# Kernel optimization log

Measured on AMD Instinct MI355X. Metric: run time of the kernel, lower is better.

Reference implementation:

```python
import jax, jax.numpy as jnp
import numpy as np

HS, FF, NH = 1024, 4096, 16
HD = HS // NH
EPS = 1e-5

def _ln(x, g, b):
    m = jnp.mean(x, axis=-1, keepdims=True)
    v = jnp.mean((x - m) ** 2, axis=-1, keepdims=True)
    return (x - m) * jax.lax.rsqrt(v + EPS) * g + b

def setup_inputs() -> dict:
    key = jax.random.key(0)
    ks = jax.random.split(key, 12)
    s = 1.0 / np.sqrt(HS)
    si = 1.0 / np.sqrt(FF)
    d = {
        "hidden_states": jax.random.normal(ks[0], (2, 2048, HS), dtype=jnp.float32),
        "attention_mask": jnp.zeros((2, 1, 1, 2048), dtype=jnp.float32),
        "Wq": jax.random.uniform(ks[1], (HS, HS), minval=-s, maxval=s),
        "bq": jnp.zeros((HS,), jnp.float32),
        "Wk": jax.random.uniform(ks[2], (HS, HS), minval=-s, maxval=s),
        "bk": jnp.zeros((HS,), jnp.float32),
        "Wv": jax.random.uniform(ks[3], (HS, HS), minval=-s, maxval=s),
        "bv": jnp.zeros((HS,), jnp.float32),
        "Wo": jax.random.uniform(ks[4], (HS, HS), minval=-s, maxval=s),
        "bo": jnp.zeros((HS,), jnp.float32),
        "W1": jax.random.uniform(ks[5], (HS, FF), minval=-s, maxval=s),
        "b1": jnp.zeros((FF,), jnp.float32),
        "W2": jax.random.uniform(ks[6], (FF, HS), minval=-si, maxval=si),
        "b2": jnp.zeros((HS,), jnp.float32),
        "ln1_g": jnp.ones((HS,), jnp.float32),
        "ln1_b": jnp.zeros((HS,), jnp.float32),
        "ln2_g": jnp.ones((HS,), jnp.float32),
        "ln2_b": jnp.zeros((HS,), jnp.float32),
    }
    return d

def reference(hidden_states, attention_mask, Wq, bq, Wk, bk, Wv, bv, Wo, bo,
              W1, b1, W2, b2, ln1_g, ln1_b, ln2_g, ln2_b):
    bs, S, _ = hidden_states.shape
    x = hidden_states
    # self-attention (dropout is identity in eval)
    q = (x @ Wq + bq).reshape(bs, S, NH, HD).transpose(0, 2, 1, 3)
    k = (x @ Wk + bk).reshape(bs, S, NH, HD).transpose(0, 2, 1, 3)
    v = (x @ Wv + bv).reshape(bs, S, NH, HD).transpose(0, 2, 1, 3)
    scores = jnp.einsum("bhqd,bhkd->bhqk", q, k) / np.sqrt(HD) + attention_mask
    probs = jax.nn.softmax(scores, axis=-1)
    attn = jnp.einsum("bhqk,bhkd->bhqd", probs, v)
    attn = attn.transpose(0, 2, 1, 3).reshape(bs, S, HS)
    mha = attn @ Wo + bo
    h = _ln(x + mha, ln1_g, ln1_b)
    # FFN
    ff = jax.nn.relu(h @ W1 + b1) @ W2 + b2
    return _ln(h + ff, ln2_g, ln2_b)
```

## Files before the change

kernel.cpp:

```cpp
#include <hip/hip_runtime.h>
#include <hip/hip_bf16.h>

#define HS   1024
#define FF   4096
#define NH   16
#define HD   64
#define SEQ  2048
#define BSZ  2
#define MROWS (BSZ * SEQ)
#define EPS  1e-5f
#define QKV_STRIDE (3 * HS)

typedef float f32x4  __attribute__((ext_vector_type(4)));
typedef short bf16x8 __attribute__((ext_vector_type(8)));

__device__ __forceinline__ unsigned short f2bf(float x) {
  unsigned int u = __float_as_uint(x);
  u += 0x7fffu + ((u >> 16) & 1u);
  return (unsigned short)(u >> 16);
}

__device__ __forceinline__ unsigned int pkbf(float a, float b) {
  union { __hip_bfloat162 h; unsigned int u; } x;
  x.h = __float22bfloat162_rn(float2{a, b});
  return x.u;
}

__device__ __forceinline__ void async16(const ushort* g, ushort* lds) {
  __builtin_amdgcn_global_load_lds(
      (const __attribute__((address_space(1))) unsigned int*)g,
      (__attribute__((address_space(3))) unsigned int*)lds, 16, 0, 0);
}

template <int TBM, int TBN, bool RELU, bool OUT_BF16, bool PARTIAL>
__global__ __launch_bounds__(256) void gemm_bf16_kernel(
    const ushort* __restrict__ A, const ushort* __restrict__ Bt,
    const float* __restrict__ bias, void* __restrict__ Cout,
    int M, int N, int K, int kLen, size_t zstride)
{
  constexpr int MI = TBM / 32;
  constexpr int NJ = TBN / 32;
  __shared__ ushort As[TBM * 64];
  __shared__ ushort Bs[TBN * 64];

  const int tid = threadIdx.x;
  const int wv = tid >> 6, ln = tid & 63;
  const int bn = blockIdx.x, bm = blockIdx.y;

  const int lr = ln & 15;
  const int lg = ln >> 4;
  const int mrow_base = (wv >> 1) * (TBM / 2);
  const int ncol_base = (wv & 1) * (TBN / 2);

  f32x4 acc[MI][NJ];
#pragma unroll
  for (int i = 0; i < MI; ++i)
#pragma unroll
    for (int j = 0; j < NJ; ++j) acc[i][j] = (f32x4){0.f, 0.f, 0.f, 0.f};

  const int rr = ln >> 3, cc = ln & 7;
  const int kBeg = blockIdx.z * kLen, kEnd = kBeg + kLen;

  for (int k0 = kBeg; k0 < kEnd; k0 += 64) {
    __syncthreads();
#pragma unroll
    for (int t = 0; t < TBM / 32; ++t) {
      const int R = wv * (TBM / 4) + t * 8 + rr;
      const int c = cc ^ (R & 7);
      async16(A + (size_t)(bm * TBM + R) * K + k0 + c * 8,
              &As[(size_t)(wv * (TBM / 4) + t * 8) * 64]);
    }
#pragma unroll
    for (int t = 0; t < TBN / 32; ++t) {
      const int R = wv * (TBN / 4) + t * 8 + rr;
      const int c = cc ^ (R & 7);
      async16(Bt + (size_t)(bn * TBN + R) * K + k0 + c * 8,
              &Bs[(size_t)(wv * (TBN / 4) + t * 8) * 64]);
    }
    __syncthreads();

#pragma unroll
    for (int s = 0; s < 2; ++s) {
      bf16x8 a[MI], b[NJ];
#pragma unroll
      for (int i = 0; i < MI; ++i) {
        const int m = mrow_base + i * 16 + lr;
        a[i] = *(const bf16x8*)&As[(size_t)m * 64 + (((s * 4 + lg) ^ (m & 7)) * 8)];
      }
#pragma unroll
      for (int j = 0; j < NJ; ++j) {
        const int n = ncol_base + j * 16 + lr;
        b[j] = *(const bf16x8*)&Bs[(size_t)n * 64 + (((s * 4 + lg) ^ (n & 7)) * 8)];
      }
#pragma unroll
      for (int i = 0; i < MI; ++i)
#pragma unroll
        for (int j = 0; j < NJ; ++j)
          acc[i][j] = __builtin_amdgcn_mfma_f32_16x16x32_bf16(a[i], b[j], acc[i][j], 0, 0, 0);
    }
  }

  const int gm0 = bm * TBM + mrow_base;
  const int gn0 = bn * TBN + ncol_base;

  if (PARTIAL) {
    float* Cp = (float*)Cout + (size_t)blockIdx.z * zstride;
#pragma unroll
    for (int i = 0; i < MI; ++i)
#pragma unroll
      for (int r = 0; r < 4; ++r) {
        const size_t row = (size_t)(gm0 + i * 16 + lg * 4 + r);
#pragma unroll
        for (int j = 0; j < NJ; ++j)
          Cp[row * N + gn0 + j * 16 + lr] = acc[i][j][r];
      }
  } else {
    float bs4[NJ];
#pragma unroll
    for (int j = 0; j < NJ; ++j) bs4[j] = bias[gn0 + j * 16 + lr];
    float* Cf = (float*)Cout;
    ushort* Cb = (ushort*)Cout;
#pragma unroll
    for (int i = 0; i < MI; ++i) {
#pragma unroll
      for (int r = 0; r < 4; ++r) {
        const size_t row = (size_t)(gm0 + i * 16 + lg * 4 + r);
#pragma unroll
        for (int j = 0; j < NJ; ++j) {
          float val = acc[i][j][r] + bs4[j];
          if (RELU) val = fmaxf(val, 0.f);
          const size_t idx = row * N + gn0 + j * 16 + lr;
          if (OUT_BF16) Cb[idx] = f2bf(val);
          else          Cf[idx] = val;
        }
      }
    }
  }
}

__device__ __forceinline__ void transpose_tile(
    const float* __restrict__ W, ushort* __restrict__ Wt,
    int K, int N, int n0, int k0, int tid, ushort (*T)[72])
{
#pragma unroll
  for (int t = 0; t < 4; ++t) {
    const int r = t * 16 + (tid >> 4);
    const int c = (tid & 15) * 4;
    const float4 w = *(const float4*)&W[(size_t)(k0 + r) * N + n0 + c];
    T[c + 0][r] = f2bf(w.x); T[c + 1][r] = f2bf(w.y);
    T[c + 2][r] = f2bf(w.z); T[c + 3][r] = f2bf(w.w);
  }
  __syncthreads();
#pragma unroll
  for (int t = 0; t < 4; ++t) {
    const int n = t * 16 + (tid >> 4);
    const int kc = (tid & 15) * 4;
    ushort4 o;
    o.x = T[n][kc]; o.y = T[n][kc + 1]; o.z = T[n][kc + 2]; o.w = T[n][kc + 3];
    *(ushort4*)&Wt[(size_t)(n0 + n) * K + k0 + kc] = o;
  }
}

__global__ __launch_bounds__(256) void prep_kernel(
    const float* __restrict__ Wq, const float* __restrict__ Wk,
    const float* __restrict__ Wv, const float* __restrict__ Wo,
    const float* __restrict__ W1, const float* __restrict__ W2,
    const float* __restrict__ bq, const float* __restrict__ bk,
    const float* __restrict__ bv, const float* __restrict__ x,
    ushort* __restrict__ Wqkvt, ushort* __restrict__ Wot,
    ushort* __restrict__ W1t, ushort* __restrict__ W2t,
    float* __restrict__ bqkv, ushort* __restrict__ xb)
{
  __shared__ ushort T[64][72];
  const int b = blockIdx.x, tid = threadIdx.x;
  const size_t M1 = 1024 * 1024;
  if (b < 1024) {
    const int w = b >> 8, l = b & 255;
    const int n0 = (l & 15) * 64, k0 = (l >> 4) * 64;
    const float* src = (w == 0) ? Wq : (w == 1) ? Wk : (w == 2) ? Wv : Wo;
    ushort* dst = (w < 3) ? (Wqkvt + (size_t)w * M1) : Wot;
    transpose_tile(src, dst, HS, HS, n0, k0, tid, T);
  } else if (b < 2048) {
    const int l = b - 1024;
    transpose_tile(W1, W1t, HS, FF, (l & 63) * 64, (l >> 6) * 64, tid, T);
  } else if (b < 3072) {
    const int l = b - 2048;
    transpose_tile(W2, W2t, FF, HS, (l & 15) * 64, (l >> 4) * 64, tid, T);
  } else if (b < 5120) {
    const size_t base = (size_t)(b - 3072) * 2048 + tid * 8;
    const float4 v0 = *(const float4*)&x[base];
    const float4 v1 = *(const float4*)&x[base + 4];
    ushort4 o0, o1;
    o0.x = f2bf(v0.x); o0.y = f2bf(v0.y); o0.z = f2bf(v0.z); o0.w = f2bf(v0.w);
    o1.x = f2bf(v1.x); o1.y = f2bf(v1.y); o1.z = f2bf(v1.z); o1.w = f2bf(v1.w);
    *(ushort4*)&xb[base] = o0;
    *(ushort4*)&xb[base + 4] = o1;
  } else {
#pragma unroll
    for (int t = 0; t < 12; ++t) {
      const int i = t * 256 + tid;
      bqkv[i] = (i < HS) ? bq[i] : (i < 2 * HS) ? bk[i - HS] : bv[i - 2 * HS];
    }
  }
}

__global__ __launch_bounds__(256) void vtrans_kernel(
    const ushort* __restrict__ vb, ushort* __restrict__ VTg, int stride)
{
  __shared__ ushort T[64][68];
  const int tid = threadIdx.x;
  const int s0 = blockIdx.x * 64;
  const int bh = blockIdx.y;
  const int b = bh >> 4, h = bh & 15;
#pragma unroll
  for (int t = 0; t < 4; ++t) {
    const int rr = t * 16 + (tid >> 4);
    const int c4 = (tid & 15) * 4;
    const ushort4 w = *(const ushort4*)&vb[(size_t)(b * SEQ + s0 + rr) * stride + h * 64 + c4];
    T[c4 + 0][rr] = w.x; T[c4 + 1][rr] = w.y;
    T[c4 + 2][rr] = w.z; T[c4 + 3][rr] = w.w;
  }
  __syncthreads();
#pragma unroll
  for (int t = 0; t < 4; ++t) {
    const int d = t * 16 + (tid >> 4);
    const int k4 = (tid & 15) * 4;
    ushort4 o;
    o.x = T[d][k4]; o.y = T[d][k4 + 1]; o.z = T[d][k4 + 2]; o.w = T[d][k4 + 3];
    *(ushort4*)&VTg[((size_t)bh * 64 + d) * SEQ + s0 + k4] = o;
  }
}

__global__ __launch_bounds__(256, 2) void attention_mfma_kernel(
    const ushort* __restrict__ Qb, const ushort* __restrict__ Kb,
    const ushort* __restrict__ VTg, const float* __restrict__ mask,
    ushort* __restrict__ O)
{
  __shared__ ushort smem[32768];
  ushort* Ks  = smem;
  ushort* VTs = smem + 8192;
  ushort* Ps  = smem + 16384;

  const int tid = threadIdx.x;
  const int wv = tid >> 6, ln = tid & 63;
  const int c = ln & 15, g = ln >> 4;
  const int qt = blockIdx.x, hh = blockIdx.y, b = blockIdx.z;
  const int bh = b * NH + hh;
  const size_t row0 = (size_t)b * SEQ + (size_t)qt * 128;
  const int ch = hh * HD;
  const int wq0 = wv * 32;

  bf16x8 qf[2][2];
#pragma unroll
  for (int nt = 0; nt < 2; ++nt)
#pragma unroll
    for (int s = 0; s < 2; ++s)
      qf[nt][s] = *(const bf16x8*)&Qb[(row0 + wq0 + nt * 16 + c) * QKV_STRIDE + ch + s * 32 + g * 8];

  f32x4 ao[4][2];
#pragma unroll
  for (int i = 0; i < 4; ++i) { ao[i][0] = (f32x4){0,0,0,0}; ao[i][1] = (f32x4){0,0,0,0}; }
  float l_r[2] = {0.f, 0.f};

  ushort* Pw = Ps + wv * 4096;
  const int rr = ln >> 3, cc = ln & 7;
  const int r4 = ln >> 4, sc = ln & 15;

  for (int kb = 0; kb < SEQ / 128; ++kb) {
    __syncthreads();
    const size_t krow0 = (size_t)b * SEQ + (size_t)kb * 128;
#pragma unroll
    for (int t = 0; t < 4; ++t) {
      const int r = wv * 32 + t * 8 + rr;
      async16(Kb + (krow0 + r) * QKV_STRIDE + ch + ((cc ^ (r & 7)) * 8),
              &Ks[(size_t)(wv * 32 + t * 8) * 64]);
    }
#pragma unroll
    for (int t = 0; t < 4; ++t) {
      const int d = wv * 16 + t * 4 + r4;
      const int srcc = (sc & 8) | ((sc & 7) ^ (d & 7));
      async16(VTg + ((size_t)bh * 64 + d) * SEQ + kb * 128 + srcc * 8,
              &VTs[(size_t)(wv * 16 + t * 4) * 128]);
    }
    __syncthreads();

    f32x4 as_[8][2];
#pragma unroll
    for (int i = 0; i < 8; ++i) { as_[i][0] = (f32x4){0,0,0,0}; as_[i][1] = (f32x4){0,0,0,0}; }
#pragma unroll
    for (int s = 0; s < 2; ++s) {
#pragma unroll
      for (int mt = 0; mt < 8; ++mt) {
        const int key = mt * 16 + c;
        const bf16x8 kf = *(const bf16x8*)&Ks[(size_t)key * 64 + (((s * 4 + g) ^ (key & 7)) * 8)];
#pragma unroll
        for (int nt = 0; nt < 2; ++nt)
          as_[mt][nt] = __builtin_amdgcn_mfma_f32_16x16x32_bf16(kf, qf[nt][s], as_[mt][nt], 0, 0, 0);
      }
    }

#pragma unroll
    for (int mt = 0; mt < 8; ++mt) {
      const float4 mk = *(const float4*)&mask[(size_t)b * SEQ + kb * 128 + mt * 16 + g * 4];
      const float mka[4] = {mk.x, mk.y, mk.z, mk.w};
#pragma unroll
      for (int nt = 0; nt < 2; ++nt) {
#pragma unroll
        for (int r = 0; r < 4; ++r) {
          const float p = __expf(fminf(as_[mt][nt][r] * 0.125f + mka[r], 60.f));
          as_[mt][nt][r] = p;
          l_r[nt] += p;
        }
      }
    }

#pragma unroll
    for (int mt = 0; mt < 8; ++mt) {
      const int kc = 2 * mt + (g >> 1);
      const int slot = (kc & 8) | ((kc & 7) ^ (c & 7));
#pragma unroll
      for (int nt = 0; nt < 2; ++nt) {
        const int q = nt * 16 + c;
        const int base = q * 128 + slot * 8 + 4 * (g & 1);
        uint2 w;
        w.x = pkbf(as_[mt][nt][0], as_[mt][nt][1]);
        w.y = pkbf(as_[mt][nt][2], as_[mt][nt][3]);
        *(uint2*)&Pw[base] = w;
      }
    }

#pragma unroll
    for (int s = 0; s < 4; ++s) {
      const int k = s * 4 + g;
      bf16x8 pf[2];
#pragma unroll
      for (int nt = 0; nt < 2; ++nt) {
        const int q = nt * 16 + c;
        const int pslot = (k & 8) | ((k & 7) ^ (q & 7));
        pf[nt] = *(const bf16x8*)&Pw[(size_t)q * 128 + pslot * 8];
      }
#pragma unroll
      for (int mt = 0; mt < 4; ++mt) {
        const int d = mt * 16 + c;
        const int vslot = (k & 8) | ((k & 7) ^ (d & 7));
        const bf16x8 vf = *(const bf16x8*)&VTs[(size_t)d * 128 + vslot * 8];
#pragma unroll
        for (int nt = 0; nt < 2; ++nt)
          ao[mt][nt] = __builtin_amdgcn_mfma_f32_16x16x32_bf16(vf, pf[nt], ao[mt][nt], 0, 0, 0);
      }
    }
  }

#pragma unroll
  for (int nt = 0; nt < 2; ++nt) {
    l_r[nt] += __shfl_xor(l_r[nt], 16, 64);
    l_r[nt] += __shfl_xor(l_r[nt], 32, 64);
  }

  __syncthreads();
  ushort* OL = smem;
#pragma unroll
  for (int nt = 0; nt < 2; ++nt) {
    const float inv = 1.f / l_r[nt];
    const int q = wq0 + nt * 16 + c;
#pragma unroll
    for (int mt = 0; mt < 4; ++mt) {
      const int d = mt * 16 + g * 4;
      uint2 w;
      w.x = pkbf(ao[mt][nt][0] * inv, ao[mt][nt][1] * inv);
      w.y = pkbf(ao[mt][nt][2] * inv, ao[mt][nt][3] * inv);
      *(uint2*)&OL[q * 72 + d] = w;
    }
  }
  __syncthreads();
#pragma unroll
  for (int it = 0; it < 4; ++it) {
    const int unit = it * 256 + tid;
    const int q = unit >> 3, sg = unit & 7;
    const uint4 w = *(const uint4*)&OL[q * 72 + sg * 8];
    *(uint4*)&O[(row0 + q) * HS + ch + sg * 8] = w;
  }
}

template <bool EMIT16>
__global__ __launch_bounds__(256) void add_ln_red_kernel(
    const float* __restrict__ P0, const float* __restrict__ P1,
    const float* __restrict__ bias, const float* __restrict__ X,
    const float* __restrict__ g, const float* __restrict__ b,
    float* __restrict__ out, ushort* __restrict__ outb)
{
  const int row = blockIdx.x;
  const int tid = threadIdx.x;
  const size_t base = (size_t)row * HS + tid * 4;
  const float4 p0 = *(const float4*)&P0[base];
  const float4 p1 = *(const float4*)&P1[base];
  const float4 bi = *(const float4*)&bias[tid * 4];
  const float4 xv = *(const float4*)&X[base];
  float4 v;
  v.x = xv.x + p0.x + p1.x + bi.x;
  v.y = xv.y + p0.y + p1.y + bi.y;
  v.z = xv.z + p0.z + p1.z + bi.z;
  v.w = xv.w + p0.w + p1.w + bi.w;
  float s1 = v.x + v.y + v.z + v.w;
  float s2 = v.x * v.x + v.y * v.y + v.z * v.z + v.w * v.w;
#pragma unroll
  for (int off = 32; off > 0; off >>= 1) {
    s1 += __shfl_down(s1, off, 64);
    s2 += __shfl_down(s2, off, 64);
  }
  __shared__ float red[8];
  __shared__ float stat[2];
  const int wid = tid >> 6;
  if ((tid & 63) == 0) { red[wid] = s1; red[4 + wid] = s2; }
  __syncthreads();
  if (tid == 0) {
    const float t1 = red[0] + red[1] + red[2] + red[3];
    const float t2 = red[4] + red[5] + red[6] + red[7];
    const float mean = t1 * (1.f / HS);
    const float var = t2 * (1.f / HS) - mean * mean;
    stat[0] = mean;
    stat[1] = rsqrtf(var + EPS);
  }
  __syncthreads();
  const float mean = stat[0], rstd = stat[1];
  const float4 gv = *(const float4*)&g[tid * 4];
  const float4 bv = *(const float4*)&b[tid * 4];
  float4 r;
  r.x = (v.x - mean) * rstd * gv.x + bv.x;
  r.y = (v.y - mean) * rstd * gv.y + bv.y;
  r.z = (v.z - mean) * rstd * gv.z + bv.z;
  r.w = (v.w - mean) * rstd * gv.w + bv.w;
  *(float4*)&out[base] = r;
  if (EMIT16) {
    ushort4 o;
    o.x = f2bf(r.x); o.y = f2bf(r.y); o.z = f2bf(r.z); o.w = f2bf(r.w);
    *(ushort4*)&outb[base] = o;
  }
}

extern "C" void kernel_launch(void* const* d_in, const int* in_sizes, int n_in,
                              void* d_out, int out_size, void* d_ws, size_t ws_size,
                              hipStream_t stream)
{
  const float* x    = (const float*)d_in[0];
  const float* mask = (const float*)d_in[1];
  const float* Wq   = (const float*)d_in[2];  const float* bq  = (const float*)d_in[3];
  const float* Wk   = (const float*)d_in[4];  const float* bk  = (const float*)d_in[5];
  const float* Wv   = (const float*)d_in[6];  const float* bv  = (const float*)d_in[7];
  const float* Wo   = (const float*)d_in[8];  const float* bo  = (const float*)d_in[9];
  const float* W1   = (const float*)d_in[10]; const float* b1  = (const float*)d_in[11];
  const float* W2   = (const float*)d_in[12]; const float* b2  = (const float*)d_in[13];
  const float* g1   = (const float*)d_in[14]; const float* be1 = (const float*)d_in[15];
  const float* g2   = (const float*)d_in[16]; const float* be2 = (const float*)d_in[17];
  float* out = (float*)d_out;

  ushort* wsu = (ushort*)d_ws;
  const size_t M1 = 1024 * 1024;

  ushort* Wqkvt = wsu;
  ushort* Wot   = wsu + 3 * M1;
  ushort* W1t   = wsu + 4 * M1;
  ushort* W2t   = wsu + 8 * M1;
  float*  bqkv  = (float*)(wsu + 12 * M1);
  ushort* xb    = wsu + 13 * M1;
  ushort* qkvb  = wsu + 17 * M1;
  ushort* VTg   = wsu + 29 * M1;
  ushort* attnb = wsu + 33 * M1;
  float*  woP   = (float*)(wsu + 13 * M1);
  float*  h     = (float*)(wsu + 29 * M1);
  ushort* hb    = wsu + 37 * M1;
  ushort* ff1o  = wsu + 13 * M1;
  float*  ff2P0 = (float*)wsu;
  float*  ff2P1 = (float*)(wsu + 39 * M1);

  const dim3 blk(256);
  const size_t SLAB = (size_t)MROWS * HS;

  prep_kernel<<<dim3(5121), blk, 0, stream>>>(
      Wq, Wk, Wv, Wo, W1, W2, bq, bk, bv, x,
      Wqkvt, Wot, W1t, W2t, bqkv, xb);

  gemm_bf16_kernel<128, 128, false, true, false><<<dim3(24, 32), blk, 0, stream>>>(
      xb, Wqkvt, bqkv, qkvb, MROWS, 3 * HS, HS, HS, 0);

  vtrans_kernel<<<dim3(SEQ / 64, BSZ * NH), blk, 0, stream>>>(qkvb + 2 * HS, VTg, QKV_STRIDE);

  attention_mfma_kernel<<<dim3(SEQ / 128, NH, BSZ), blk, 0, stream>>>(
      qkvb, qkvb + HS, VTg, mask, attnb);

  gemm_bf16_kernel<64, 128, false, false, true><<<dim3(8, 64, 2), blk, 0, stream>>>(
      attnb, Wot, nullptr, woP, MROWS, HS, HS, HS / 2, SLAB);
  add_ln_red_kernel<true><<<dim3(MROWS), blk, 0, stream>>>(
      woP, woP + SLAB, bo, x, g1, be1, h, hb);

  gemm_bf16_kernel<128, 128, true, true, false><<<dim3(32, 32), blk, 0, stream>>>(
      hb, W1t, b1, ff1o, MROWS, FF, HS, HS, 0);
  gemm_bf16_kernel<128, 128, false, false, true><<<dim3(8, 32, 2), blk, 0, stream>>>(
      ff1o, W2t, nullptr, ff2P0, MROWS, HS, FF, FF / 2, (size_t)(ff2P1 - ff2P0));
  add_ln_red_kernel<false><<<dim3(MROWS), blk, 0, stream>>>(
      ff2P0, ff2P1, b2, h, g2, be2, out, nullptr);
}
```

Baseline: 390.4 us.

## Double-buffer K/V tiles, stage mask in LDS, build P fragments via permlane swaps

The attention kernel now double-buffers the K and V^T tiles in shared memory. It prefetches the next key block with async loads and waits using a partial vmcnt, so global loads overlap with the MFMA compute. The mask row is loaded into LDS once, and the P matrix is rearranged into MFMA operand layout in registers with permlane32/16 swaps instead of a round trip through shared memory. s_setprio hints are placed around the MFMA sections. LDS use grows, which may limit occupancy, and the fragment mapping from permlane must match the old P layout exactly.

```diff
diff --git a/kernel.cpp b/kernel.cpp
--- a/kernel.cpp
+++ b/kernel.cpp
@@ -236,10 +236,8 @@
     const ushort* __restrict__ VTg, const float* __restrict__ mask,
     ushort* __restrict__ O)
 {
-  __shared__ ushort smem[32768];
-  ushort* Ks  = smem;
-  ushort* VTs = smem + 8192;
-  ushort* Ps  = smem + 16384;
+  __shared__ ushort smem[36864];
+  float* mL = (float*)(smem + 32768);
 
   const int tid = threadIdx.x;
   const int wv = tid >> 6, ln = tid & 63;
@@ -257,17 +255,18 @@
     for (int s = 0; s < 2; ++s)
       qf[nt][s] = *(const bf16x8*)&Qb[(row0 + wq0 + nt * 16 + c) * QKV_STRIDE + ch + s * 32 + g * 8];
 
-  f32x4 ao[4][2];
-#pragma unroll
-  for (int i = 0; i < 4; ++i) { ao[i][0] = (f32x4){0,0,0,0}; ao[i][1] = (f32x4){0,0,0,0}; }
-  float l_r[2] = {0.f, 0.f};
-
-  ushort* Pw = Ps + wv * 4096;
+  const float* mrow = mask + (size_t)b * SEQ;
+#pragma unroll
+  for (int t = 0; t < 2; ++t)
+    async16((const ushort*)(mrow + t * 1024 + wv * 256 + ln * 4),
+            (ushort*)(mL + t * 1024 + wv * 256));
+
   const int rr = ln >> 3, cc = ln & 7;
   const int r4 = ln >> 4, sc = ln & 15;
 
-  for (int kb = 0; kb < SEQ / 128; ++kb) {
-    __syncthreads();
+  auto stage = [&](int kb, int bsel) {
+    ushort* Ks  = smem + bsel * 16384;
+    ushort* VTs = Ks + 8192;
     const size_t krow0 = (size_t)b * SEQ + (size_t)kb * 128;
 #pragma unroll
     for (int t = 0; t < 4; ++t) {
@@ -282,11 +281,35 @@
       async16(VTg + ((size_t)bh * 64 + d) * SEQ + kb * 128 + srcc * 8,
               &VTs[(size_t)(wv * 16 + t * 4) * 128]);
     }
-    __syncthreads();
+  };
+
+  f32x4 ao[4][2];
+#pragma unroll
+  for (int i = 0; i < 4; ++i) { ao[i][0] = (f32x4){0,0,0,0}; ao[i][1] = (f32x4){0,0,0,0}; }
+  float l_r[2] = {0.f, 0.f};
+
+  stage(0, 0);
+
+  for (int kb = 0; kb < SEQ / 128; ++kb) {
+    const int cur = kb & 1;
+    __builtin_amdgcn_s_barrier();
+    __builtin_amdgcn_sched_barrier(0);
+    if (kb + 1 < SEQ / 128) {
+      stage(kb + 1, cur ^ 1);
+      asm volatile("s_waitcnt vmcnt(8)" ::: "memory");
+    } else {
+      asm volatile("s_waitcnt vmcnt(0)" ::: "memory");
+    }
+    __builtin_amdgcn_s_barrier();
+    __builtin_amdgcn_sched_barrier(0);
+
+    ushort* Ks  = smem + cur * 16384;
+    ushort* VTs = Ks + 8192;
 
     f32x4 as_[8][2];
 #pragma unroll
     for (int i = 0; i < 8; ++i) { as_[i][0] = (f32x4){0,0,0,0}; as_[i][1] = (f32x4){0,0,0,0}; }
+    __builtin_amdgcn_s_setprio(1);
 #pragma unroll
     for (int s = 0; s < 2; ++s) {
 #pragma unroll
@@ -298,10 +321,11 @@
           as_[mt][nt] = __builtin_amdgcn_mfma_f32_16x16x32_bf16(kf, qf[nt][s], as_[mt][nt], 0, 0, 0);
       }
     }
+    __builtin_amdgcn_s_setprio(0);
 
 #pragma unroll
     for (int mt = 0; mt < 8; ++mt) {
-      const float4 mk = *(const float4*)&mask[(size_t)b * SEQ + kb * 128 + mt * 16 + g * 4];
+      const float4 mk = *(const float4*)&mL[kb * 128 + mt * 16 + g * 4];
       const float mka[4] = {mk.x, mk.y, mk.z, mk.w};
 #pragma unroll
       for (int nt = 0; nt < 2; ++nt) {
@@ -315,39 +339,34 @@
     }
 
 #pragma unroll
-    for (int mt = 0; mt < 8; ++mt) {
-      const int kc = 2 * mt + (g >> 1);
-      const int slot = (kc & 8) | ((kc & 7) ^ (c & 7));
+    for (int s = 0; s < 4; ++s) {
+      bf16x8 pf[2];
 #pragma unroll
       for (int nt = 0; nt < 2; ++nt) {
-        const int q = nt * 16 + c;
-        const int base = q * 128 + slot * 8 + 4 * (g & 1);
-        uint2 w;
-        w.x = pkbf(as_[mt][nt][0], as_[mt][nt][1]);
-        w.y = pkbf(as_[mt][nt][2], as_[mt][nt][3]);
-        *(uint2*)&Pw[base] = w;
-      }
-    }
-
-#pragma unroll
-    for (int s = 0; s < 4; ++s) {
-      const int k = s * 4 + g;
-      bf16x8 pf[2];
-#pragma unroll
-      for (int nt = 0; nt < 2; ++nt) {
-        const int q = nt * 16 + c;
-        const int pslot = (k & 8) | ((k & 7) ^ (q & 7));
-        pf[nt] = *(const bf16x8*)&Pw[(size_t)q * 128 + pslot * 8];
-      }
+        const unsigned A0 = pkbf(as_[2 * s][nt][0], as_[2 * s][nt][1]);
+        const unsigned A1 = pkbf(as_[2 * s][nt][2], as_[2 * s][nt][3]);
+        const unsigned B0 = pkbf(as_[2 * s + 1][nt][0], as_[2 * s + 1][nt][1]);
+        const unsigned B1 = pkbf(as_[2 * s + 1][nt][2], as_[2 * s + 1][nt][3]);
+        auto x0 = __builtin_amdgcn_permlane32_swap(A0, B0, false, false);
+        auto x1 = __builtin_amdgcn_permlane32_swap(A1, B1, false, false);
+        auto y0 = __builtin_amdgcn_permlane16_swap(x0[0], x0[1], false, false);
+        auto y1 = __builtin_amdgcn_permlane16_swap(x1[0], x1[1], false, false);
+        union { unsigned w[4]; bf16x8 v; } u;
+        u.w[0] = y0[0]; u.w[1] = y1[0]; u.w[2] = y0[1]; u.w[3] = y1[1];
+        pf[nt] = u.v;
+      }
+      __builtin_amdgcn_s_setprio(1);
 #pragma unroll
       for (int mt = 0; mt < 4; ++mt) {
         const int d = mt * 16 + c;
+        const int k = s * 4 + g;
         const int vslot = (k & 8) | ((k & 7) ^ (d & 7));
         const bf16x8 vf = *(const bf16x8*)&VTs[(size_t)d * 128 + vslot * 8];
 #pragma unroll
         for (int nt = 0; nt < 2; ++nt)
           ao[mt][nt] = __builtin_amdgcn_mfma_f32_16x16x32_bf16(vf, pf[nt], ao[mt][nt], 0, 0, 0);
       }
+      __builtin_amdgcn_s_setprio(0);
     }
   }
 
```

After: 383.6 us. No clear change (-1.7%).
